# Optimization experiments

Hardware: AMD Instinct MI355X
Metric: run time of the kernel (lower is better)

## Reference

```python
import jax, jax.numpy as jnp
import numpy as np

B, S, D, H, FF = 16, 1024, 1024, 8, 4096
DH = D // H
EPS = 1e-5

def _ln(x, g, b):
    mu = jnp.mean(x, axis=-1, keepdims=True)
    var = jnp.mean((x - mu) ** 2, axis=-1, keepdims=True)
    return (x - mu) * jax.lax.rsqrt(var + EPS) * g + b

def setup_inputs() -> dict:
    key = jax.random.key(0)
    ks = jax.random.split(key, 12)
    sd = D ** -0.5
    return {
        "x": jax.random.normal(ks[0], (B, S, D), jnp.float32),
        "bias": jax.random.normal(ks[1], (S, S), jnp.float32),
        "Wq": jax.random.normal(ks[2], (D, D), jnp.float32) * sd,
        "bq": jnp.zeros((D,), jnp.float32),
        "Wk": jax.random.normal(ks[3], (D, D), jnp.float32) * sd,
        "bk": jnp.zeros((D,), jnp.float32),
        "Wv": jax.random.normal(ks[4], (D, D), jnp.float32) * sd,
        "bv": jnp.zeros((D,), jnp.float32),
        "Wo": jax.random.normal(ks[5], (D, D), jnp.float32) * sd,
        "bo": jnp.zeros((D,), jnp.float32),
        "ln1_g": jnp.ones((D,), jnp.float32),
        "ln1_b": jnp.zeros((D,), jnp.float32),
        "W1": jax.random.normal(ks[6], (FF, D), jnp.float32) * sd,
        "b1": jnp.zeros((FF,), jnp.float32),
        "W2": jax.random.normal(ks[7], (D, FF), jnp.float32) * (FF ** -0.5),
        "b2": jnp.zeros((D,), jnp.float32),
        "ln2_g": jnp.ones((D,), jnp.float32),
        "ln2_b": jnp.zeros((D,), jnp.float32),
    }

def reference(x, bias, Wq, bq, Wk, bk, Wv, bv, Wo, bo, ln1_g, ln1_b,
              W1, b1, W2, b2, ln2_g, ln2_b):
    # torch nn.Linear: y = x @ W.T + b
    Q = x @ Wq.T + bq  # [B,S,D]
    K = x @ Wk.T + bk
    V = x @ Wv.T + bv
    # Faithful to torch: plain row-major reshape [B,S,H*dh] -> [B*H,S,dh]
    Q = Q.reshape(B * H, S, DH)
    K = K.reshape(B * H, S, DH)
    V = V.reshape(B * H, S, DH)
    scale = DH ** -0.5
    scores = jnp.einsum('bqd,bkd->bqk', Q, K)  # [B*H,S,S]
    scores = (scores + bias[None]) * scale      # bias added BEFORE scaling, as in source
    attn = jax.nn.softmax(scores, axis=-1)
    selfattention = attn[0]
    ctx = jnp.einsum('bqk,bkd->bqd', attn, V).reshape(B, S, D)
    out = ctx @ Wo.T + bo
    out = _ln(out + x, ln1_g, ln1_b)
    # FFN
    h = jax.nn.relu(out @ W1.T + b1)
    ff = h @ W2.T + b2
    out2 = _ln(ff + out, ln2_g, ln2_b)
    return out2, selfattention
```

## Files before the change

kernel.cpp:

```cpp
#include <hip/hip_runtime.h>
#include <hip/hip_bf16.h>
#include <math.h>

typedef __attribute__((ext_vector_type(4))) float f32x4;
typedef __attribute__((ext_vector_type(8))) __bf16 bf16x8;
typedef __attribute__((ext_vector_type(4))) __bf16 bf16x4;

static constexpr float SCALE = 0.08838834764831845f;
static constexpr float SCALE_LOG2E = 0.1275174482f;

__device__ __forceinline__ void load_lds16(const void* g, void* l) {
  __builtin_amdgcn_global_load_lds(
      (const __attribute__((address_space(1))) void*)g,
      (__attribute__((address_space(3))) void*)l, 16, 0, 0);
}

__global__ __launch_bounds__(256) void cast_kernel(const float* __restrict__ s,
                                                   __bf16* __restrict__ d, int n4) {
  int i = blockIdx.x * blockDim.x + threadIdx.x;
  int stride = gridDim.x * blockDim.x;
  for (; i < n4; i += stride) {
    float4 v = reinterpret_cast<const float4*>(s)[i];
    bf16x4 o;
    o[0] = (__bf16)v.x; o[1] = (__bf16)v.y; o[2] = (__bf16)v.z; o[3] = (__bf16)v.w;
    reinterpret_cast<bf16x4*>(d)[i] = o;
  }
}

__global__ __launch_bounds__(256) void cast_weights(
    const float* __restrict__ wq, const float* __restrict__ wk,
    const float* __restrict__ wv, const float* __restrict__ wo,
    const float* __restrict__ w1, const float* __restrict__ w2,
    __bf16* __restrict__ dq, __bf16* __restrict__ dk,
    __bf16* __restrict__ dv, __bf16* __restrict__ dwo,
    __bf16* __restrict__ d1, __bf16* __restrict__ d2) {
  int i = blockIdx.x * blockDim.x + threadIdx.x;
  int stride = gridDim.x * blockDim.x;
  for (; i < 3145728; i += stride) {
    const float* s; __bf16* d; int j;
    if (i < 262144)       { s = wq; d = dq;  j = i; }
    else if (i < 524288)  { s = wk; d = dk;  j = i - 262144; }
    else if (i < 786432)  { s = wv; d = dv;  j = i - 524288; }
    else if (i < 1048576) { s = wo; d = dwo; j = i - 786432; }
    else if (i < 2097152) { s = w1; d = d1;  j = i - 1048576; }
    else                  { s = w2; d = d2;  j = i - 2097152; }
    float4 v = reinterpret_cast<const float4*>(s)[j];
    bf16x4 o;
    o[0] = (__bf16)v.x; o[1] = (__bf16)v.y; o[2] = (__bf16)v.z; o[3] = (__bf16)v.w;
    reinterpret_cast<bf16x4*>(d)[j] = o;
  }
}

__global__ __launch_bounds__(256) void scale_cast_kernel(const float* __restrict__ s,
                                                         __bf16* __restrict__ d, int n4) {
  int i = blockIdx.x * blockDim.x + threadIdx.x;
  int stride = gridDim.x * blockDim.x;
  for (; i < n4; i += stride) {
    float4 v = reinterpret_cast<const float4*>(s)[i];
    bf16x4 o;
    o[0] = (__bf16)(v.x * SCALE_LOG2E); o[1] = (__bf16)(v.y * SCALE_LOG2E);
    o[2] = (__bf16)(v.z * SCALE_LOG2E); o[3] = (__bf16)(v.w * SCALE_LOG2E);
    reinterpret_cast<bf16x4*>(d)[i] = o;
  }
}

template <int EPI>
__global__ __launch_bounds__(512, 2) void gemm_bt(
    const __bf16* __restrict__ A, const __bf16* __restrict__ Bw,
    const float* __restrict__ bvec, __bf16* __restrict__ Cb,
    float* __restrict__ Cf, int M, int N, int K) {
  __shared__ __align__(16) char sm[131072];

  const int ntn = N >> 8;
  const int nwg = gridDim.x;
  const int bid = blockIdx.x;
  const int b = (bid & 7) * (nwg >> 3) + (bid >> 3);
  const int tm = b / ntn, tn = b % ntn;
  const int t = threadIdx.x, lane = t & 63;
  const int w = t >> 6;
  const int wm = w >> 2, wn = w & 3;
  const int l15 = lane & 15, lq = lane >> 4;

  f32x4 acc[8][4] = {};

  const int r0 = t >> 3;
  const int r1 = r0 + 64;
  const int kb0 = (((t & 7) << 4) ^ ((r0 & 7) << 4));
  const int wbase = w << 10;

  auto stage = [&](int kt, int p) {
    char* base = sm + (p << 16);
    const size_t kofs = (size_t)(kb0 >> 1) + ((size_t)kt << 6);
#pragma unroll
    for (int h = 0; h < 2; ++h) {
      const __bf16* gA = A + (size_t)((tm << 8) + (h << 7) + r0) * K + kofs;
      const __bf16* gA2 = A + (size_t)((tm << 8) + (h << 7) + r1) * K + kofs;
      char* lA = base + (h << 14) + wbase;
      load_lds16(gA, lA);
      load_lds16(gA2, lA + 8192);
      const __bf16* gB = Bw + (size_t)((tn << 8) + (h << 7) + r0) * K + kofs;
      const __bf16* gB2 = Bw + (size_t)((tn << 8) + (h << 7) + r1) * K + kofs;
      char* lB = base + 32768 + (h << 14) + wbase;
      load_lds16(gB, lB);
      load_lds16(gB2, lB + 8192);
    }
  };

  stage(0, 0);
  __syncthreads();

  const int NT = K >> 6;
  const int rbB = (wn & 1) << 6;
  for (int kt = 0; kt < NT; ++kt) {
    const int p = kt & 1;
    const char* Ab = sm + (p << 16) + (wm << 14);
    const char* Bb = sm + (p << 16) + 32768 + ((wn >> 1) << 14);
    if (kt + 1 < NT) stage(kt + 1, p ^ 1);

    bf16x8 bfv[4][2];
#pragma unroll
    for (int nf = 0; nf < 4; ++nf) {
      const int r = rbB + (nf << 4) + l15;
      const int sw = (r & 7) << 4;
#pragma unroll
      for (int ks = 0; ks < 2; ++ks) {
        const int lb = (ks << 6) + (lq << 4);
        bfv[nf][ks] = *(const bf16x8*)(Bb + r * 128 + (lb ^ sw));
      }
    }
#pragma unroll
    for (int q = 0; q < 4; ++q) {
      bf16x8 af[2][2];
#pragma unroll
      for (int dm = 0; dm < 2; ++dm) {
        const int r = (((q << 1) + dm) << 4) + l15;
        const int sw = (r & 7) << 4;
#pragma unroll
        for (int ks = 0; ks < 2; ++ks) {
          const int lb = (ks << 6) + (lq << 4);
          af[dm][ks] = *(const bf16x8*)(Ab + r * 128 + (lb ^ sw));
        }
      }
#pragma unroll
      for (int ks = 0; ks < 2; ++ks)
#pragma unroll
        for (int dm = 0; dm < 2; ++dm)
#pragma unroll
          for (int nf = 0; nf < 4; ++nf)
            acc[(q << 1) + dm][nf] = __builtin_amdgcn_mfma_f32_16x16x32_bf16(
                af[dm][ks], bfv[nf][ks], acc[(q << 1) + dm][nf], 0, 0, 0);
    }
    __syncthreads();
  }

  const int row0 = (tm << 8) + (wm << 7) + (lq << 2);
  const int col0 = (tn << 8) + (wn << 6) + l15;
#pragma unroll
  for (int nf = 0; nf < 4; ++nf) {
    const int col = col0 + (nf << 4);
    const float bv = bvec[col];
#pragma unroll
    for (int mf = 0; mf < 8; ++mf) {
#pragma unroll
      for (int r = 0; r < 4; ++r) {
        const int row = row0 + (mf << 4) + r;
        float v = acc[mf][nf][r] + bv;
        if (EPI == 1) v = fmaxf(v, 0.f);
        if (EPI == 2) {
          Cf[(size_t)row * N + col] = v;
        } else if (EPI == 3) {
          size_t vt = ((size_t)(row >> 7) << 17) + ((size_t)(col & 127) << 10) +
                      ((row & 127) << 3) + (col >> 7);
          Cb[vt] = (__bf16)v;
        } else {
          Cb[(size_t)row * N + col] = (__bf16)v;
        }
      }
    }
  }
}

__global__ __launch_bounds__(256) void attn_flash(
    const __bf16* __restrict__ Q, const __bf16* __restrict__ K,
    const __bf16* __restrict__ VT, const __bf16* __restrict__ biasS,
    __bf16* __restrict__ ctx) {
  __shared__ __bf16 Ks[64 * 128];
  __shared__ __bf16 VTs[128 * 64];
  __shared__ __bf16 Ps[4][16 * 64];

  const int bid = blockIdx.x;
  const int b = ((bid & 7) << 8) | (bid >> 3);
  const int g = b >> 4;
  const int q0 = (b & 15) << 6;
  const size_t goff = (size_t)g << 17;
  const __bf16* Qg = Q + goff;
  const __bf16* Kg = K + goff;
  const __bf16* VTg = VT + goff;

  const int t = threadIdx.x, w = t >> 6, lane = t & 63;
  const int l15 = lane & 15, lq = lane >> 4;
  const int qg = q0 + (w << 4) + l15;

  bf16x8 qf[4];
  {
    const __bf16* qrow = Qg + (size_t)qg * 128 + (lq << 3);
#pragma unroll
    for (int ec = 0; ec < 4; ++ec) qf[ec] = *(const bf16x8*)(qrow + (ec << 5));
  }
  const __bf16* bSr = biasS + ((size_t)qg << 10) + (lq << 2);

  float mrun = -INFINITY, lrun = 0.f;
  f32x4 cacc[8] = {};

  for (int kb = 0; kb < 1024; kb += 64) {
    {
      int srow = lane >> 4;
      int sbo = (lane & 15) << 4;
#pragma unroll
      for (int i = 0; i < 4; ++i) {
        int c = (w << 2) + i;
        int r = (c << 2) + srow;
        int ke = (sbo ^ ((r & 7) << 4)) >> 1;
        load_lds16(Kg + (size_t)(kb + r) * 128 + ke, (char*)Ks + (c << 10));
      }
    }
    {
      int srow = lane >> 3;
      int sbo = (lane & 7) << 4;
#pragma unroll
      for (int i = 0; i < 4; ++i) {
        int c = (w << 2) + i;
        int e = (c << 3) + srow;
        int ke = kb + ((sbo ^ ((e & 7) << 4)) >> 1);
        load_lds16(VTg + (size_t)e * 1024 + ke, (char*)VTs + (c << 10));
      }
    }
    __syncthreads();

    f32x4 sacc[4] = {};
#pragma unroll
    for (int ec = 0; ec < 4; ++ec) {
      const int lb = (ec << 6) + (lq << 4);
#pragma unroll
      for (int kn = 0; kn < 4; ++kn) {
        int rb = (kn << 4) + l15;
        bf16x8 kf = *(const bf16x8*)((const char*)Ks + rb * 256 + (lb ^ ((rb & 7) << 4)));
        sacc[kn] = __builtin_amdgcn_mfma_f32_16x16x32_bf16(kf, qf[ec], sacc[kn], 0, 0, 0);
      }
    }

    float sv[4][4];
    const __bf16* bt = bSr + kb;
#pragma unroll
    for (int kn = 0; kn < 4; ++kn) {
      bf16x4 bb = *(const bf16x4*)(bt + (kn << 4));
#pragma unroll
      for (int r = 0; r < 4; ++r)
        sv[kn][r] = fmaf(sacc[kn][r], SCALE_LOG2E, (float)bb[r]);
    }
    float mt = sv[0][0];
#pragma unroll
    for (int kn = 0; kn < 4; ++kn)
#pragma unroll
      for (int r = 0; r < 4; ++r) mt = fmaxf(mt, sv[kn][r]);
    mt = fmaxf(mt, __shfl_xor(mt, 16));
    mt = fmaxf(mt, __shfl_xor(mt, 32));

    float mnew = fmaxf(mrun, mt);
    float alpha = exp2f(mrun - mnew);
    mrun = mnew;
    float alphaR[4];
#pragma unroll
    for (int r = 0; r < 4; ++r)
      alphaR[r] = __shfl(alpha, (lane & 48) + ((lane & 48) >> 2) + r);
#pragma unroll
    for (int et = 0; et < 8; ++et)
#pragma unroll
      for (int r = 0; r < 4; ++r) cacc[et][r] *= alphaR[r];

    float psum = 0.f;
#pragma unroll
    for (int kn = 0; kn < 4; ++kn)
#pragma unroll
      for (int r = 0; r < 4; ++r) {
        float p = exp2f(sv[kn][r] - mrun);
        sv[kn][r] = p;
        psum += p;
      }
    psum += __shfl_xor(psum, 16);
    psum += __shfl_xor(psum, 32);
    lrun = lrun * alpha + psum;

#pragma unroll
    for (int kn = 0; kn < 4; ++kn) {
      bf16x4 pk;
      pk[0] = (__bf16)sv[kn][0]; pk[1] = (__bf16)sv[kn][1];
      pk[2] = (__bf16)sv[kn][2]; pk[3] = (__bf16)sv[kn][3];
      int bo = (kn << 5) + (lq << 3);
      *(bf16x4*)((char*)Ps[w] + l15 * 128 + (bo ^ ((l15 & 7) << 4))) = pk;
    }
    asm volatile("s_waitcnt lgkmcnt(0)" ::: "memory");
    __builtin_amdgcn_sched_barrier(0);

#pragma unroll
    for (int ks = 0; ks < 2; ++ks) {
      const int lb = (ks << 6) + (lq << 4);
      bf16x8 paf = *(const bf16x8*)((const char*)Ps[w] + l15 * 128 + (lb ^ ((l15 & 7) << 4)));
#pragma unroll
      for (int et = 0; et < 8; ++et) {
        int e = (et << 4) + l15;
        bf16x8 vf = *(const bf16x8*)((const char*)VTs + e * 128 + (lb ^ ((e & 7) << 4)));
        cacc[et] = __builtin_amdgcn_mfma_f32_16x16x32_bf16(paf, vf, cacc[et], 0, 0, 0);
      }
    }
    __syncthreads();
  }

  float lrunR[4];
#pragma unroll
  for (int r = 0; r < 4; ++r)
    lrunR[r] = __shfl(lrun, (lane & 48) + ((lane & 48) >> 2) + r);
  __bf16* cg = ctx + goff;
  const int qr = q0 + (w << 4) + (lq << 2);
#pragma unroll
  for (int et = 0; et < 8; ++et)
#pragma unroll
    for (int r = 0; r < 4; ++r) {
      float v = cacc[et][r] / lrunR[r];
      cg[(size_t)(qr + r) * 128 + (et << 4) + l15] = (__bf16)v;
    }
}

__global__ __launch_bounds__(256) void attn_head0(
    const __bf16* __restrict__ Q, const __bf16* __restrict__ K,
    const float* __restrict__ bias, float* __restrict__ out) {
  __shared__ float qrow[128];
  __shared__ float red[8];
  const int q = blockIdx.x, t = threadIdx.x;
  if (t < 128) qrow[t] = (float)Q[(size_t)q * 128 + t];
  __syncthreads();
  float s[4];
#pragma unroll
  for (int c = 0; c < 4; ++c) {
    int kc = (c << 8) + t;
    const __bf16* kr = K + (size_t)kc * 128;
    float dot = 0.f;
#pragma unroll
    for (int e = 0; e < 128; e += 8) {
      bf16x8 kv = *(const bf16x8*)(kr + e);
#pragma unroll
      for (int j = 0; j < 8; ++j) dot += qrow[e + j] * (float)kv[j];
    }
    s[c] = (dot + bias[(size_t)q * 1024 + kc]) * SCALE;
  }
  float mx = fmaxf(fmaxf(s[0], s[1]), fmaxf(s[2], s[3]));
#pragma unroll
  for (int d = 32; d >= 1; d >>= 1) mx = fmaxf(mx, __shfl_xor(mx, d));
  const int w = t >> 6, lane = t & 63;
  if (lane == 0) red[w] = mx;
  __syncthreads();
  mx = fmaxf(fmaxf(red[0], red[1]), fmaxf(red[2], red[3]));
  float ex[4], sum = 0.f;
#pragma unroll
  for (int c = 0; c < 4; ++c) { ex[c] = __expf(s[c] - mx); sum += ex[c]; }
#pragma unroll
  for (int d = 32; d >= 1; d >>= 1) sum += __shfl_xor(sum, d);
  __syncthreads();
  if (lane == 0) red[4 + w] = sum;
  __syncthreads();
  sum = red[4] + red[5] + red[6] + red[7];
  float inv = 1.f / sum;
#pragma unroll
  for (int c = 0; c < 4; ++c) out[(size_t)q * 1024 + (c << 8) + t] = ex[c] * inv;
}

template <int B_BF16>
__global__ __launch_bounds__(256) void ln_res(
    const float* __restrict__ a, const void* __restrict__ bptr,
    const float* __restrict__ gam, const float* __restrict__ bet,
    float* __restrict__ outf, __bf16* __restrict__ outb) {
  __shared__ float red[8];
  const int row = blockIdx.x, t = threadIdx.x;
  const size_t base = (size_t)row << 10;
  float4 va = reinterpret_cast<const float4*>(a + base)[t];
  float b0, b1, b2, b3;
  if (B_BF16) {
    bf16x4 vb = reinterpret_cast<const bf16x4*>((const __bf16*)bptr + base)[t];
    b0 = (float)vb[0]; b1 = (float)vb[1]; b2 = (float)vb[2]; b3 = (float)vb[3];
  } else {
    float4 vb = reinterpret_cast<const float4*>((const float*)bptr + base)[t];
    b0 = vb.x; b1 = vb.y; b2 = vb.z; b3 = vb.w;
  }
  float v0 = va.x + b0, v1 = va.y + b1, v2 = va.z + b2, v3 = va.w + b3;
  float s = v0 + v1 + v2 + v3;
  float qq = v0 * v0 + v1 * v1 + v2 * v2 + v3 * v3;
#pragma unroll
  for (int d = 32; d >= 1; d >>= 1) {
    s += __shfl_xor(s, d);
    qq += __shfl_xor(qq, d);
  }
  const int w = t >> 6, lane = t & 63;
  if (lane == 0) { red[w] = s; red[4 + w] = qq; }
  __syncthreads();
  s = red[0] + red[1] + red[2] + red[3];
  qq = red[4] + red[5] + red[6] + red[7];
  const float mu = s * (1.f / 1024.f);
  const float var = qq * (1.f / 1024.f) - mu * mu;
  const float rs = rsqrtf(var + 1e-5f);
  float4 g4 = reinterpret_cast<const float4*>(gam)[t];
  float4 b4 = reinterpret_cast<const float4*>(bet)[t];
  float o0 = (v0 - mu) * rs * g4.x + b4.x;
  float o1 = (v1 - mu) * rs * g4.y + b4.y;
  float o2 = (v2 - mu) * rs * g4.z + b4.z;
  float o3 = (v3 - mu) * rs * g4.w + b4.w;
  if (outf) reinterpret_cast<float4*>(outf + base)[t] = make_float4(o0, o1, o2, o3);
  if (outb) {
    bf16x4 ob;
    ob[0] = (__bf16)o0; ob[1] = (__bf16)o1; ob[2] = (__bf16)o2; ob[3] = (__bf16)o3;
    reinterpret_cast<bf16x4*>(outb + base)[t] = ob;
  }
}

extern "C" void kernel_launch(void* const* d_in, const int* in_sizes, int n_in,
                              void* d_out, int out_size, void* d_ws, size_t ws_size,
                              hipStream_t stream) {
  (void)in_sizes; (void)n_in; (void)out_size; (void)ws_size;
  const float* x    = (const float*)d_in[0];
  const float* bias = (const float*)d_in[1];
  const float* Wq   = (const float*)d_in[2];
  const float* bq   = (const float*)d_in[3];
  const float* Wk   = (const float*)d_in[4];
  const float* bk   = (const float*)d_in[5];
  const float* Wv   = (const float*)d_in[6];
  const float* bv   = (const float*)d_in[7];
  const float* Wo   = (const float*)d_in[8];
  const float* bo   = (const float*)d_in[9];
  const float* g1   = (const float*)d_in[10];
  const float* b1l  = (const float*)d_in[11];
  const float* W1   = (const float*)d_in[12];
  const float* b1f  = (const float*)d_in[13];
  const float* W2   = (const float*)d_in[14];
  const float* b2f  = (const float*)d_in[15];
  const float* g2   = (const float*)d_in[16];
  const float* b2l  = (const float*)d_in[17];

  char* ws = (char*)d_ws;
  size_t off = 0;
  auto alloc = [&](size_t bytes) {
    char* p = ws + off;
    off += (bytes + 255) & ~(size_t)255;
    return p;
  };
  __bf16* wqb  = (__bf16*)alloc(2097152);
  __bf16* wkb  = (__bf16*)alloc(2097152);
  __bf16* wvb  = (__bf16*)alloc(2097152);
  __bf16* wob  = (__bf16*)alloc(2097152);
  __bf16* w1b  = (__bf16*)alloc(8388608);
  __bf16* w2b  = (__bf16*)alloc(8388608);
  __bf16* biasS = (__bf16*)alloc(2097152);
  __bf16* xb   = (__bf16*)alloc(33554432);
  __bf16* Qb   = (__bf16*)alloc(4ull * 33554432);
  __bf16* Kb   = Qb + 16777216;
  __bf16* VTb  = Kb + 16777216;
  __bf16* ctxb = VTb + 16777216;
  __bf16* hb   = Qb;
  __bf16* res1b = xb;

  float* out2     = (float*)d_out;
  float* selfattn = (float*)d_out + 16777216;
  float* attn_out = out2;
  float* ff       = out2;

  cast_kernel<<<2048, 256, 0, stream>>>(x, xb, 16777216 / 4);
  cast_weights<<<2048, 256, 0, stream>>>(Wq, Wk, Wv, Wo, W1, W2,
                                         wqb, wkb, wvb, wob, w1b, w2b);
  scale_cast_kernel<<<512, 256, 0, stream>>>(bias, biasS, 1048576 / 4);

  gemm_bt<0><<<64 * 4, 512, 0, stream>>>(xb, wqb, bq, Qb, nullptr, 16384, 1024, 1024);
  gemm_bt<0><<<64 * 4, 512, 0, stream>>>(xb, wkb, bk, Kb, nullptr, 16384, 1024, 1024);
  gemm_bt<3><<<64 * 4, 512, 0, stream>>>(xb, wvb, bv, VTb, nullptr, 16384, 1024, 1024);

  attn_head0<<<1024, 256, 0, stream>>>(Qb, Kb, bias, selfattn);
  attn_flash<<<128 * 16, 256, 0, stream>>>(Qb, Kb, VTb, biasS, ctxb);

  gemm_bt<2><<<64 * 4, 512, 0, stream>>>(ctxb, wob, bo, nullptr, attn_out, 16384, 1024, 1024);

  ln_res<0><<<16384, 256, 0, stream>>>(attn_out, x, g1, b1l, nullptr, res1b);

  gemm_bt<1><<<64 * 16, 512, 0, stream>>>(res1b, w1b, b1f, hb, nullptr, 16384, 4096, 1024);
  gemm_bt<2><<<64 * 4, 512, 0, stream>>>(hb, w2b, b2f, nullptr, ff, 16384, 1024, 4096);

  ln_res<1><<<16384, 256, 0, stream>>>(ff, res1b, g2, b2l, out2, nullptr);
}
```

Measured before the change: 771.4 us.

## Retile GEMM to 256x128 with triple-buffered LDS pipeline and MFMA priority hints

The GEMM tile shrinks from 256x256 to 256x128 with a 4x2 wave layout, which doubles the grid size. LDS moves to a three-stage ring, and the per-iteration __syncthreads is replaced by an explicit vmcnt wait plus barrier, so loads run two K-steps ahead. The attention kernel raises wave priority around its MFMA blocks with s_setprio. The aim is better latency hiding and more workgroups per GEMM, at the cost of lower reuse per tile and occupancy of one block per CU because of the larger shared-memory footprint.

```diff
diff --git a/kernel.cpp b/kernel.cpp
--- a/kernel.cpp
+++ b/kernel.cpp
@@ -65,62 +65,66 @@
 }
 
 template <int EPI>
-__global__ __launch_bounds__(512, 2) void gemm_bt(
+__global__ __launch_bounds__(512, 1) void gemm_bt(
     const __bf16* __restrict__ A, const __bf16* __restrict__ Bw,
     const float* __restrict__ bvec, __bf16* __restrict__ Cb,
     float* __restrict__ Cf, int M, int N, int K) {
-  __shared__ __align__(16) char sm[131072];
-
-  const int ntn = N >> 8;
+  __shared__ __align__(16) char sm[147456];
+
+  const int ntn = N >> 7;
   const int nwg = gridDim.x;
   const int bid = blockIdx.x;
   const int b = (bid & 7) * (nwg >> 3) + (bid >> 3);
   const int tm = b / ntn, tn = b % ntn;
   const int t = threadIdx.x, lane = t & 63;
   const int w = t >> 6;
-  const int wm = w >> 2, wn = w & 3;
+  const int wm = w >> 1, wn = w & 1;
   const int l15 = lane & 15, lq = lane >> 4;
 
-  f32x4 acc[8][4] = {};
-
-  const int r0 = t >> 3;
-  const int r1 = r0 + 64;
-  const int kb0 = (((t & 7) << 4) ^ ((r0 & 7) << 4));
-  const int wbase = w << 10;
-
-  auto stage = [&](int kt, int p) {
-    char* base = sm + (p << 16);
-    const size_t kofs = (size_t)(kb0 >> 1) + ((size_t)kt << 6);
-#pragma unroll
-    for (int h = 0; h < 2; ++h) {
-      const __bf16* gA = A + (size_t)((tm << 8) + (h << 7) + r0) * K + kofs;
-      const __bf16* gA2 = A + (size_t)((tm << 8) + (h << 7) + r1) * K + kofs;
-      char* lA = base + (h << 14) + wbase;
-      load_lds16(gA, lA);
-      load_lds16(gA2, lA + 8192);
-      const __bf16* gB = Bw + (size_t)((tn << 8) + (h << 7) + r0) * K + kofs;
-      const __bf16* gB2 = Bw + (size_t)((tn << 8) + (h << 7) + r1) * K + kofs;
-      char* lB = base + 32768 + (h << 14) + wbase;
-      load_lds16(gB, lB);
-      load_lds16(gB2, lB + 8192);
+  f32x4 acc[4][4] = {};
+
+  const int srow = lane >> 3;
+  const int sbo = (lane & 7) << 4;
+  const int keSwz = (sbo ^ (srow << 4)) >> 1;
+  const size_t aBase = (size_t)(tm << 8) * K;
+  const size_t bBase = (size_t)(tn << 7) * K;
+
+  auto stage = [&](int kt, int bf) {
+    char* base = sm + bf * 49152;
+    const size_t ke = (size_t)keSwz + ((size_t)kt << 6);
+#pragma unroll
+    for (int i = 0; i < 4; ++i) {
+      int c = (w << 2) + i;
+      int r = (c << 3) + srow;
+      load_lds16(A + aBase + (size_t)r * K + ke, base + (c << 10));
+    }
+#pragma unroll
+    for (int i = 0; i < 2; ++i) {
+      int c = (w << 1) + i;
+      int r = (c << 3) + srow;
+      load_lds16(Bw + bBase + (size_t)r * K + ke, base + 32768 + (c << 10));
     }
   };
 
+  const int NT = K >> 6;
   stage(0, 0);
-  __syncthreads();
-
-  const int NT = K >> 6;
-  const int rbB = (wn & 1) << 6;
+  stage(1, 1);
+
+  int rb = 0, sb = 2;
   for (int kt = 0; kt < NT; ++kt) {
-    const int p = kt & 1;
-    const char* Ab = sm + (p << 16) + (wm << 14);
-    const char* Bb = sm + (p << 16) + 32768 + ((wn >> 1) << 14);
-    if (kt + 1 < NT) stage(kt + 1, p ^ 1);
+    if (kt + 1 < NT)
+      asm volatile("s_waitcnt vmcnt(6)\ns_barrier" ::: "memory");
+    else
+      asm volatile("s_waitcnt vmcnt(0)\ns_barrier" ::: "memory");
+    if (kt + 2 < NT) stage(kt + 2, sb);
+
+    const char* Ab = sm + rb * 49152;
+    const char* Bb = Ab + 32768;
 
     bf16x8 bfv[4][2];
 #pragma unroll
     for (int nf = 0; nf < 4; ++nf) {
-      const int r = rbB + (nf << 4) + l15;
+      const int r = (wn << 6) + (nf << 4) + l15;
       const int sw = (r & 7) << 4;
 #pragma unroll
       for (int ks = 0; ks < 2; ++ks) {
@@ -129,38 +133,34 @@
       }
     }
 #pragma unroll
-    for (int q = 0; q < 4; ++q) {
-      bf16x8 af[2][2];
-#pragma unroll
-      for (int dm = 0; dm < 2; ++dm) {
-        const int r = (((q << 1) + dm) << 4) + l15;
-        const int sw = (r & 7) << 4;
-#pragma unroll
-        for (int ks = 0; ks < 2; ++ks) {
-          const int lb = (ks << 6) + (lq << 4);
-          af[dm][ks] = *(const bf16x8*)(Ab + r * 128 + (lb ^ sw));
-        }
+    for (int mf = 0; mf < 4; ++mf) {
+      bf16x8 af[2];
+      const int r = (wm << 6) + (mf << 4) + l15;
+      const int sw = (r & 7) << 4;
+#pragma unroll
+      for (int ks = 0; ks < 2; ++ks) {
+        const int lb = (ks << 6) + (lq << 4);
+        af[ks] = *(const bf16x8*)(Ab + r * 128 + (lb ^ sw));
       }
 #pragma unroll
       for (int ks = 0; ks < 2; ++ks)
 #pragma unroll
-        for (int dm = 0; dm < 2; ++dm)
-#pragma unroll
-          for (int nf = 0; nf < 4; ++nf)
-            acc[(q << 1) + dm][nf] = __builtin_amdgcn_mfma_f32_16x16x32_bf16(
-                af[dm][ks], bfv[nf][ks], acc[(q << 1) + dm][nf], 0, 0, 0);
-    }
-    __syncthreads();
-  }
-
-  const int row0 = (tm << 8) + (wm << 7) + (lq << 2);
-  const int col0 = (tn << 8) + (wn << 6) + l15;
+        for (int nf = 0; nf < 4; ++nf)
+          acc[mf][nf] = __builtin_amdgcn_mfma_f32_16x16x32_bf16(
+              af[ks], bfv[nf][ks], acc[mf][nf], 0, 0, 0);
+    }
+    rb = (rb == 2) ? 0 : rb + 1;
+    sb = (sb == 2) ? 0 : sb + 1;
+  }
+
+  const int row0 = (tm << 8) + (wm << 6) + (lq << 2);
+  const int col0 = (tn << 7) + (wn << 6) + l15;
 #pragma unroll
   for (int nf = 0; nf < 4; ++nf) {
     const int col = col0 + (nf << 4);
     const float bv = bvec[col];
 #pragma unroll
-    for (int mf = 0; mf < 8; ++mf) {
+    for (int mf = 0; mf < 4; ++mf) {
 #pragma unroll
       for (int r = 0; r < 4; ++r) {
         const int row = row0 + (mf << 4) + r;
@@ -238,6 +238,7 @@
     __syncthreads();
 
     f32x4 sacc[4] = {};
+    __builtin_amdgcn_s_setprio(1);
 #pragma unroll
     for (int ec = 0; ec < 4; ++ec) {
       const int lb = (ec << 6) + (lq << 4);
@@ -248,6 +249,7 @@
         sacc[kn] = __builtin_amdgcn_mfma_f32_16x16x32_bf16(kf, qf[ec], sacc[kn], 0, 0, 0);
       }
     }
+    __builtin_amdgcn_s_setprio(0);
 
     float sv[4][4];
     const __bf16* bt = bSr + kb;
@@ -302,6 +304,7 @@
     asm volatile("s_waitcnt lgkmcnt(0)" ::: "memory");
     __builtin_amdgcn_sched_barrier(0);
 
+    __builtin_amdgcn_s_setprio(1);
 #pragma unroll
     for (int ks = 0; ks < 2; ++ks) {
       const int lb = (ks << 6) + (lq << 4);
@@ -313,6 +316,7 @@
         cacc[et] = __builtin_amdgcn_mfma_f32_16x16x32_bf16(paf, vf, cacc[et], 0, 0, 0);
       }
     }
+    __builtin_amdgcn_s_setprio(0);
     __syncthreads();
   }
 
@@ -476,19 +480,19 @@
                                          wqb, wkb, wvb, wob, w1b, w2b);
   scale_cast_kernel<<<512, 256, 0, stream>>>(bias, biasS, 1048576 / 4);
 
-  gemm_bt<0><<<64 * 4, 512, 0, stream>>>(xb, wqb, bq, Qb, nullptr, 16384, 1024, 1024);
-  gemm_bt<0><<<64 * 4, 512, 0, stream>>>(xb, wkb, bk, Kb, nullptr, 16384, 1024, 1024);
-  gemm_bt<3><<<64 * 4, 512, 0, stream>>>(xb, wvb, bv, VTb, nullptr, 16384, 1024, 1024);
+  gemm_bt<0><<<64 * 8, 512, 0, stream>>>(xb, wqb, bq, Qb, nullptr, 16384, 1024, 1024);
+  gemm_bt<0><<<64 * 8, 512, 0, stream>>>(xb, wkb, bk, Kb, nullptr, 16384, 1024, 1024);
+  gemm_bt<3><<<64 * 8, 512, 0, stream>>>(xb, wvb, bv, VTb, nullptr, 16384, 1024, 1024);
 
   attn_head0<<<1024, 256, 0, stream>>>(Qb, Kb, bias, selfattn);
   attn_flash<<<128 * 16, 256, 0, stream>>>(Qb, Kb, VTb, biasS, ctxb);
 
-  gemm_bt<2><<<64 * 4, 512, 0, stream>>>(ctxb, wob, bo, nullptr, attn_out, 16384, 1024, 1024);
+  gemm_bt<2><<<64 * 8, 512, 0, stream>>>(ctxb, wob, bo, nullptr, attn_out, 16384, 1024, 1024);
 
   ln_res<0><<<16384, 256, 0, stream>>>(attn_out, x, g1, b1l, nullptr, res1b);
 
-  gemm_bt<1><<<64 * 16, 512, 0, stream>>>(res1b, w1b, b1f, hb, nullptr, 16384, 4096, 1024);
-  gemm_bt<2><<<64 * 4, 512, 0, stream>>>(hb, w2b, b2f, nullptr, ff, 16384, 1024, 4096);
+  gemm_bt<1><<<64 * 32, 512, 0, stream>>>(res1b, w1b, b1f, hb, nullptr, 16384, 4096, 1024);
+  gemm_bt<2><<<64 * 8, 512, 0, stream>>>(hb, w2b, b2f, nullptr, ff, 16384, 1024, 4096);
 
   ln_res<1><<<16384, 256, 0, stream>>>(ff, res1b, g2, b2l, out2, nullptr);
 }
```

Result: slower. 815.4 us (+5.7%).

## Add double-buffered ping-pong GEMM for FFN and raise MFMA priority in attention

Applied to the files above, without the earlier changes.

Introduces a new gemm8p kernel using 128KB LDS double buffering, half-tile staging interleaved with MFMA phases, explicit vmcnt waits and s_setprio around MFMA blocks, and uses it for both FFN GEMMs. It also wraps the attention kernel's MFMA loops in s_setprio. The aim is to overlap global-to-LDS loads with matrix math and cut barrier stalls in the largest GEMMs. Occupancy drops to one block per CU, and the ReLU is removed from the old gemm_bt epilogue, though that path no longer uses it.

```diff
diff --git a/kernel.cpp b/kernel.cpp
--- a/kernel.cpp
+++ b/kernel.cpp
@@ -165,7 +165,6 @@
       for (int r = 0; r < 4; ++r) {
         const int row = row0 + (mf << 4) + r;
         float v = acc[mf][nf][r] + bv;
-        if (EPI == 1) v = fmaxf(v, 0.f);
         if (EPI == 2) {
           Cf[(size_t)row * N + col] = v;
         } else if (EPI == 3) {
@@ -180,6 +179,161 @@
   }
 }
 
+template <int EPI>
+__global__ __launch_bounds__(512, 1) void gemm8p(
+    const __bf16* __restrict__ A, const __bf16* __restrict__ Bw,
+    const float* __restrict__ bvec, __bf16* __restrict__ Cb,
+    float* __restrict__ Cf, int M, int N, int K) {
+  __shared__ __align__(16) char sm[131072];
+
+  const int ntn = N >> 8;
+  const int nwg = gridDim.x;
+  const int bid = blockIdx.x;
+  const int b = (bid & 7) * (nwg >> 3) + (bid >> 3);
+  const int tm = b / ntn, tn = b % ntn;
+  const int t = threadIdx.x, lane = t & 63;
+  const int w = t >> 6;
+  const int wm = w >> 2, wn = w & 3;
+  const int l15 = lane & 15, lq = lane >> 4;
+
+  f32x4 acc[8][4] = {};
+
+  int rr[2], keS[2], dstoff[2];
+#pragma unroll
+  for (int rd = 0; rd < 2; ++rd) {
+    int o = (w << 10) + (lane << 4) + (rd << 13);
+    int q = o >> 7, sub = (o >> 6) & 1, s = (o >> 4) & 3;
+    rr[rd] = 2 * q + sub;
+    keS[rd] = ((s ^ (q & 3)) << 4) >> 1;
+    dstoff[rd] = (w << 10) + (rd << 13);
+  }
+
+  auto stageH = [&](const __bf16* Mp, int baseRow, int kofs, char* region) {
+#pragma unroll
+    for (int rd = 0; rd < 2; ++rd)
+      load_lds16(Mp + (size_t)(baseRow + rr[rd]) * K + kofs + keS[rd],
+                 region + dstoff[rd]);
+  };
+
+  auto rdoff = [&](int r) {
+    return ((r >> 1) << 7) + ((r & 1) << 6) + ((lq ^ ((r >> 1) & 3)) << 4);
+  };
+
+  const int aRow = tm << 8, bRow = tn << 8;
+  const int NT = K >> 6;
+
+  stageH(A, aRow, 0, sm);
+  stageH(Bw, bRow, 0, sm + 32768);
+  stageH(A, aRow, 32, sm + 16384);
+  stageH(Bw, bRow, 32, sm + 49152);
+
+  for (int kt = 0; kt < NT; ++kt) {
+    const int p = kt & 1;
+    char* cur = sm + (p << 16);
+    char* nxt = sm + ((p ^ 1) << 16);
+    const bool more = (kt + 1 < NT);
+    const int kn0 = (kt + 1) << 6;
+
+    bf16x8 bfv[4], af[4];
+
+    asm volatile("s_waitcnt vmcnt(4)\ns_barrier" ::: "memory");
+#pragma unroll
+    for (int nf = 0; nf < 4; ++nf)
+      bfv[nf] = *(const bf16x8*)(cur + 32768 + rdoff((wn << 6) + (nf << 4) + l15));
+#pragma unroll
+    for (int mf = 0; mf < 4; ++mf)
+      af[mf] = *(const bf16x8*)(cur + rdoff((wm << 7) + (mf << 4) + l15));
+    if (more) stageH(A, aRow, kn0, nxt);
+    asm volatile("s_waitcnt lgkmcnt(0)" ::: "memory");
+    __builtin_amdgcn_sched_barrier(0);
+    __builtin_amdgcn_s_setprio(1);
+#pragma unroll
+    for (int mf = 0; mf < 4; ++mf)
+#pragma unroll
+      for (int nf = 0; nf < 4; ++nf)
+        acc[mf][nf] = __builtin_amdgcn_mfma_f32_16x16x32_bf16(
+            af[mf], bfv[nf], acc[mf][nf], 0, 0, 0);
+    __builtin_amdgcn_s_setprio(0);
+    __builtin_amdgcn_sched_barrier(0);
+
+#pragma unroll
+    for (int mf = 0; mf < 4; ++mf)
+      af[mf] = *(const bf16x8*)(cur + rdoff((wm << 7) + ((mf + 4) << 4) + l15));
+    if (more) stageH(Bw, bRow, kn0, nxt + 32768);
+    asm volatile("s_waitcnt lgkmcnt(0)" ::: "memory");
+    __builtin_amdgcn_sched_barrier(0);
+    __builtin_amdgcn_s_setprio(1);
+#pragma unroll
+    for (int mf = 0; mf < 4; ++mf)
+#pragma unroll
+      for (int nf = 0; nf < 4; ++nf)
+        acc[mf + 4][nf] = __builtin_amdgcn_mfma_f32_16x16x32_bf16(
+            af[mf], bfv[nf], acc[mf + 4][nf], 0, 0, 0);
+    __builtin_amdgcn_s_setprio(0);
+    __builtin_amdgcn_sched_barrier(0);
+
+    if (more)
+      asm volatile("s_waitcnt vmcnt(4)\ns_barrier" ::: "memory");
+    else
+      asm volatile("s_waitcnt vmcnt(0)\ns_barrier" ::: "memory");
+#pragma unroll
+    for (int nf = 0; nf < 4; ++nf)
+      bfv[nf] = *(const bf16x8*)(cur + 49152 + rdoff((wn << 6) + (nf << 4) + l15));
+#pragma unroll
+    for (int mf = 0; mf < 4; ++mf)
+      af[mf] = *(const bf16x8*)(cur + 16384 + rdoff((wm << 7) + (mf << 4) + l15));
+    if (more) stageH(A, aRow, kn0 + 32, nxt + 16384);
+    asm volatile("s_waitcnt lgkmcnt(0)" ::: "memory");
+    __builtin_amdgcn_sched_barrier(0);
+    __builtin_amdgcn_s_setprio(1);
+#pragma unroll
+    for (int mf = 0; mf < 4; ++mf)
+#pragma unroll
+      for (int nf = 0; nf < 4; ++nf)
+        acc[mf][nf] = __builtin_amdgcn_mfma_f32_16x16x32_bf16(
+            af[mf], bfv[nf], acc[mf][nf], 0, 0, 0);
+    __builtin_amdgcn_s_setprio(0);
+    __builtin_amdgcn_sched_barrier(0);
+
+#pragma unroll
+    for (int mf = 0; mf < 4; ++mf)
+      af[mf] = *(const bf16x8*)(cur + 16384 + rdoff((wm << 7) + ((mf + 4) << 4) + l15));
+    if (more) stageH(Bw, bRow, kn0 + 32, nxt + 49152);
+    asm volatile("s_waitcnt lgkmcnt(0)" ::: "memory");
+    __builtin_amdgcn_sched_barrier(0);
+    __builtin_amdgcn_s_setprio(1);
+#pragma unroll
+    for (int mf = 0; mf < 4; ++mf)
+#pragma unroll
+      for (int nf = 0; nf < 4; ++nf)
+        acc[mf + 4][nf] = __builtin_amdgcn_mfma_f32_16x16x32_bf16(
+            af[mf], bfv[nf], acc[mf + 4][nf], 0, 0, 0);
+    __builtin_amdgcn_s_setprio(0);
+    __builtin_amdgcn_sched_barrier(0);
+  }
+
+  const int row0 = (tm << 8) + (wm << 7) + (lq << 2);
+  const int col0 = (tn << 8) + (wn << 6) + l15;
+#pragma unroll
+  for (int nf = 0; nf < 4; ++nf) {
+    const int col = col0 + (nf << 4);
+    const float bv = bvec[col];
+#pragma unroll
+    for (int mf = 0; mf < 8; ++mf) {
+#pragma unroll
+      for (int r = 0; r < 4; ++r) {
+        const int row = row0 + (mf << 4) + r;
+        float v = acc[mf][nf][r] + bv;
+        if (EPI == 1) v = fmaxf(v, 0.f);
+        if (EPI == 2)
+          Cf[(size_t)row * N + col] = v;
+        else
+          Cb[(size_t)row * N + col] = (__bf16)v;
+      }
+    }
+  }
+}
+
 __global__ __launch_bounds__(256) void attn_flash(
     const __bf16* __restrict__ Q, const __bf16* __restrict__ K,
     const __bf16* __restrict__ VT, const __bf16* __restrict__ biasS,
@@ -238,6 +392,7 @@
     __syncthreads();
 
     f32x4 sacc[4] = {};
+    __builtin_amdgcn_s_setprio(1);
 #pragma unroll
     for (int ec = 0; ec < 4; ++ec) {
       const int lb = (ec << 6) + (lq << 4);
@@ -248,6 +403,7 @@
         sacc[kn] = __builtin_amdgcn_mfma_f32_16x16x32_bf16(kf, qf[ec], sacc[kn], 0, 0, 0);
       }
     }
+    __builtin_amdgcn_s_setprio(0);
 
     float sv[4][4];
     const __bf16* bt = bSr + kb;
@@ -302,6 +458,7 @@
     asm volatile("s_waitcnt lgkmcnt(0)" ::: "memory");
     __builtin_amdgcn_sched_barrier(0);
 
+    __builtin_amdgcn_s_setprio(1);
 #pragma unroll
     for (int ks = 0; ks < 2; ++ks) {
       const int lb = (ks << 6) + (lq << 4);
@@ -313,6 +470,7 @@
         cacc[et] = __builtin_amdgcn_mfma_f32_16x16x32_bf16(paf, vf, cacc[et], 0, 0, 0);
       }
     }
+    __builtin_amdgcn_s_setprio(0);
     __syncthreads();
   }
 
@@ -487,8 +645,8 @@
 
   ln_res<0><<<16384, 256, 0, stream>>>(attn_out, x, g1, b1l, nullptr, res1b);
 
-  gemm_bt<1><<<64 * 16, 512, 0, stream>>>(res1b, w1b, b1f, hb, nullptr, 16384, 4096, 1024);
-  gemm_bt<2><<<64 * 4, 512, 0, stream>>>(hb, w2b, b2f, nullptr, ff, 16384, 1024, 4096);
+  gemm8p<1><<<64 * 16, 512, 0, stream>>>(res1b, w1b, b1f, hb, nullptr, 16384, 4096, 1024);
+  gemm8p<2><<<64 * 4, 512, 0, stream>>>(hb, w2b, b2f, nullptr, ff, 16384, 1024, 4096);
 
   ln_res<1><<<16384, 256, 0, stream>>>(ff, res1b, g2, b2l, out2, nullptr);
 }
```

Measured after the change: 788.3 us. +2.2%, slower.
